# Performance work log

Hardware: AMD Instinct MI355X
Metric: run time of the kernel (lower is better)

The kernel has to match this reference:

```python
import jax, jax.numpy as jnp
import numpy as np

ALPHA = 2.0
BETA = 50.0
BASE = 0.5
MARGIN = 0.1

B, D = 8192, 128
NUM_CLASSES = 512


def setup_inputs() -> dict:
    key = jax.random.key(0)
    k1, k2 = jax.random.split(key)
    emb = jax.random.normal(k1, (B, D), dtype=jnp.float32)
    emb = emb / jnp.linalg.norm(emb, axis=1, keepdims=True)  # unit-norm embeddings (standard for MS loss)
    labels = jax.random.randint(k2, (B,), 0, NUM_CLASSES, dtype=jnp.int64)
    return {"emb": emb, "labels": labels}


def reference(emb, labels):
    # sim: [B, B] similarity matrix
    sim = emb @ emb.T
    n = emb.shape[0]
    eq = labels[:, None] == labels[None, :]
    eye = jnp.eye(n, dtype=bool)
    pos = eq & ~eye          # positive pairs, diagonal removed
    neg = ~eq                # negative pairs

    # per-row hard-mining thresholds
    pos_min = jnp.min(jnp.where(pos, sim, jnp.inf), axis=1)    # min positive sim per row
    neg_max = jnp.max(jnp.where(neg, sim, -jnp.inf), axis=1)   # max negative sim per row

    neg_hard = neg & (sim + MARGIN > pos_min[:, None])
    pos_hard = pos & (sim - MARGIN < neg_max[:, None])

    # fallback: if mining selects nothing in a row, use all pos/neg (matches torch code)
    neg_sel = jnp.where(jnp.any(neg_hard, axis=1, keepdims=True), neg_hard, neg)
    pos_sel = jnp.where(jnp.any(pos_hard, axis=1, keepdims=True), pos_hard, pos)

    pos_loss = jnp.log1p(jnp.sum(jnp.where(pos_sel, jnp.exp(-ALPHA * (sim - BASE)), 0.0), axis=1)) / ALPHA
    neg_loss = jnp.log1p(jnp.sum(jnp.where(neg_sel, jnp.exp(BETA * (sim - BASE)), 0.0), axis=1)) / BETA

    valid = jnp.any(pos, axis=1) & jnp.any(neg, axis=1)  # rows skipped in torch loop
    row_loss = pos_loss + neg_loss
    num_valid = jnp.maximum(jnp.sum(valid.astype(jnp.float32)), 1.0)
    return jnp.sum(jnp.where(valid, row_loss, 0.0)) / num_valid
```

## Files before the change

kernel.cpp:

```cpp
#include <hip/hip_runtime.h>
#include <hip/hip_bf16.h>

#define NROW 8192
#define NDIM 128
#define CTILE 64
#define CCHUNK 8
#define RBLK 128
#define CAP 64
#define NCLS 512

typedef __attribute__((ext_vector_type(8))) short short8;
typedef __attribute__((ext_vector_type(4))) float f32x4;
typedef __attribute__((address_space(1))) const unsigned int guint;
typedef __attribute__((address_space(3))) unsigned int luint;

__device__ __forceinline__ unsigned f2u_mono(float f) {
  unsigned u = __float_as_uint(f);
  return (u & 0x80000000u) ? ~u : (u | 0x80000000u);
}
__device__ __forceinline__ float u2f_mono(unsigned u) {
  return __uint_as_float((u & 0x80000000u) ? (u ^ 0x80000000u) : ~u);
}
__device__ __forceinline__ unsigned short f2bf(float f) {
  unsigned u = __float_as_uint(f);
  u += 0x7fffu + ((u >> 16) & 1u);
  return (unsigned short)(u >> 16);
}

__global__ __launch_bounds__(256) void k_convert(const float* __restrict__ e,
                                                 unsigned short* __restrict__ h,
                                                 const int* __restrict__ labels,
                                                 unsigned* __restrict__ cls_cnt,
                                                 int* __restrict__ cls_list) {
  const int gid = blockIdx.x * 256 + threadIdx.x;
  if (gid < NROW) {
    const int c = labels[gid];
    const unsigned idx = atomicAdd(&cls_cnt[c], 1u);
    if (idx < CAP) cls_list[c * CAP + idx] = gid;
  }
  int i = gid * 8;
  float4 f0 = *reinterpret_cast<const float4*>(e + i);
  float4 f1 = *reinterpret_cast<const float4*>(e + i + 4);
  ushort4 a, b;
  a.x = f2bf(f0.x); a.y = f2bf(f0.y); a.z = f2bf(f0.z); a.w = f2bf(f0.w);
  b.x = f2bf(f1.x); b.y = f2bf(f1.y); b.z = f2bf(f1.z); b.w = f2bf(f1.w);
  *reinterpret_cast<ushort4*>(h + i) = a;
  *reinterpret_cast<ushort4*>(h + i + 4) = b;
}

__global__ __launch_bounds__(256) void k_pos1(
    const float* __restrict__ emb, const unsigned* __restrict__ cls_cnt,
    const int* __restrict__ cls_list, float* __restrict__ pmin,
    float* __restrict__ apb, float* __restrict__ pcache) {
  __shared__ float Le[CAP][NDIM + 1];
  __shared__ int rows_s[CAP];
  const int c = blockIdx.x;
  const int t = threadIdx.x;
  const int cnt = (int)min(cls_cnt[c], (unsigned)CAP);
  if (cnt == 0) return;
  if (t < cnt) rows_s[t] = cls_list[c * CAP + t];
  __syncthreads();
  for (int idx = t; idx < cnt * NDIM; idx += 256) {
    const int k = idx >> 7, d = idx & 127;
    Le[k][d] = emb[(size_t)rows_s[k] * NDIM + d];
  }
  __syncthreads();

  const int il = t >> 4, jl = t & 15;
  for (int ib = 0; ib < cnt; ib += 16) {
    const int i = ib + il;
    float pm = INFINITY, apv = 0.f;
    for (int jb = 0; jb < cnt; jb += 16) {
      const int j = jb + jl;
      float p = INFINITY;
      if (i < cnt && j < cnt) {
        if (i != j) {
          float s = 0.f;
#pragma unroll 8
          for (int d = 0; d < NDIM; ++d) s = fmaf(Le[i][d], Le[j][d], s);
          p = s;
        }
        pcache[(size_t)rows_s[i] * CAP + j] = p;
        if (i != j) {
          pm = fminf(pm, p);
          apv += exp2f(fmaf(p, -2.885390082f, 1.442695041f));
        }
      }
    }
    pm = fminf(pm, __shfl_xor(pm, 1)); pm = fminf(pm, __shfl_xor(pm, 2));
    pm = fminf(pm, __shfl_xor(pm, 4)); pm = fminf(pm, __shfl_xor(pm, 8));
    apv += __shfl_xor(apv, 1); apv += __shfl_xor(apv, 2);
    apv += __shfl_xor(apv, 4); apv += __shfl_xor(apv, 8);
    if (jl == 0 && i < cnt) {
      pmin[rows_s[i]] = pm;
      apb[rows_s[i]] = apv;
    }
  }
}

__device__ __forceinline__ void stage_tile(const unsigned short* __restrict__ eh,
                                           int colBase, int t,
                                           unsigned short* __restrict__ Lbuf) {
#pragma unroll
  for (int it = 0; it < 4; ++it) {
    const int idx = it * 256 + t;
    const int r = idx >> 4;
    const int c = idx & 15;
    const int q = c ^ (r & 15);
    const unsigned short* src = eh + (size_t)(colBase + r) * NDIM + q * 8;
    unsigned short* dst = Lbuf + r * NDIM + c * 8;
    __builtin_amdgcn_global_load_lds((guint*)src, (luint*)dst, 16, 0, 0);
  }
}

__device__ __forceinline__ void mfma_from_lds(const unsigned short* __restrict__ Lbuf,
                                              const short8 (&bv)[4][2],
                                              const f32x4& Z,
                                              int g, int l15,
                                              f32x4 (&acc)[4][2]) {
#pragma unroll
  for (int kk = 0; kk < 4; ++kk) {
    short8 av[4];
#pragma unroll
    for (int m = 0; m < 4; ++m) {
      const int R = m * 16 + l15;
      const int pc = (kk * 4 + g) ^ l15;
      av[m] = *reinterpret_cast<const short8*>(Lbuf + R * NDIM + pc * 8);
    }
#pragma unroll
    for (int m = 0; m < 4; ++m)
#pragma unroll
      for (int n = 0; n < 2; ++n)
        acc[m][n] = __builtin_amdgcn_mfma_f32_16x16x32_bf16(
            av[m], bv[kk][n], (kk == 0) ? Z : acc[m][n], 0, 0, 0);
  }
}

__global__ __launch_bounds__(256, 3) void k_neg(
    const unsigned short* __restrict__ eh, const int* __restrict__ labels,
    const float* __restrict__ pmin, unsigned* __restrict__ nmaxu,
    float* __restrict__ anb, float* __restrict__ hnb) {
  __shared__ unsigned short L[2][CTILE * NDIM];

  const int t = threadIdx.x;
  const int lane = t & 63;
  const int wid = t >> 6;
  const int g = lane >> 4;
  const int l15 = lane & 15;
  const int rowBase = blockIdx.y * RBLK;
  const int col0 = blockIdx.x * CCHUNK * CTILE;

  stage_tile(eh, col0, t, L[0]);

  short8 bv[4][2];
  int lr[2];
  float thrn[2];
#pragma unroll
  for (int n = 0; n < 2; ++n) {
    const int grow = rowBase + wid * 32 + n * 16 + l15;
    lr[n] = labels[grow];
    thrn[n] = pmin[grow] - 0.1f;
#pragma unroll
    for (int kk = 0; kk < 4; ++kk)
      bv[kk][n] = *reinterpret_cast<const short8*>(eh + (size_t)grow * NDIM + kk * 32 + g * 8);
  }

  float nmaxA[2] = {-INFINITY, -INFINITY};
  float anA[2] = {0.f, 0.f}, hnA[2] = {0.f, 0.f};
  const f32x4 Z = {0.f, 0.f, 0.f, 0.f};

  asm volatile("s_waitcnt vmcnt(0)");
  __syncthreads();

  f32x4 acc[4][2];
  int cur = 0;
  for (int tt = 0; tt < CCHUNK; ++tt) {
    const int colBase = col0 + tt * CTILE;
    if (tt + 1 < CCHUNK) stage_tile(eh, colBase + CTILE, t, L[cur ^ 1]);
    int4 lcv[4];
#pragma unroll
    for (int m = 0; m < 4; ++m)
      lcv[m] = *reinterpret_cast<const int4*>(labels + colBase + m * 16 + g * 4);
    mfma_from_lds(L[cur], bv, Z, g, l15, acc);
#pragma unroll
    for (int n = 0; n < 2; ++n) {
#pragma unroll
      for (int m = 0; m < 4; ++m) {
#pragma unroll
        for (int r = 0; r < 4; ++r) {
          const float s = acc[m][n][r];
          const int lc = (r == 0) ? lcv[m].x : (r == 1) ? lcv[m].y
                        : (r == 2) ? lcv[m].z : lcv[m].w;
          const float x = (lr[n] == lc) ? -INFINITY : s;
          nmaxA[n] = fmaxf(nmaxA[n], x);
          const float e = exp2f(fmaf(x, 72.13475205f, -36.06737602f));
          anA[n] += e;
          hnA[n] += (x > thrn[n]) ? e : 0.f;
        }
      }
    }
    asm volatile("s_waitcnt vmcnt(0)");
    __syncthreads();
    cur ^= 1;
  }

#pragma unroll
  for (int n = 0; n < 2; ++n) {
    const int grow = rowBase + wid * 32 + n * 16 + l15;
    float nm = nmaxA[n], a0 = anA[n], a1 = hnA[n];
    nm = fmaxf(nm, __shfl_xor(nm, 16)); nm = fmaxf(nm, __shfl_xor(nm, 32));
    a0 += __shfl_xor(a0, 16); a0 += __shfl_xor(a0, 32);
    a1 += __shfl_xor(a1, 16); a1 += __shfl_xor(a1, 32);
    if (g == 0 && nm > -INFINITY) atomicMax(&nmaxu[grow], f2u_mono(nm));
    if (g == 1 && a0 > 0.f) atomicAdd(&anb[grow], a0);
    if (g == 2 && a1 > 0.f) atomicAdd(&hnb[grow], a1);
  }
}

__global__ __launch_bounds__(256) void k_final(
    const int* __restrict__ labels, const unsigned* __restrict__ cls_cnt,
    const unsigned* __restrict__ nmaxu, const float* __restrict__ pcache,
    const float* __restrict__ apb, const float* __restrict__ anb,
    const float* __restrict__ hnb, float* __restrict__ partial,
    unsigned* __restrict__ done, float* __restrict__ out) {
  const int t = threadIdx.x;
  const int row = blockIdx.x * 256 + t;
  const int c = labels[row];
  const int cnt = (int)min(cls_cnt[c], (unsigned)CAP);
  const float thrp = u2f_mono(nmaxu[row]) + 0.1f;
  float hp = 0.f;
  for (int j = 0; j < cnt; ++j) {
    const float p = pcache[(size_t)row * CAP + j];
    hp += (p < thrp) ? exp2f(fmaf(p, -2.885390082f, 1.442695041f)) : 0.f;
  }
  const float ap = apb[row], an = anb[row], hn = hnb[row];
  const bool valid = (ap > 0.f) && (an > 0.f);
  const float ps = (hp > 0.f) ? hp : ap;
  const float ns = (hn > 0.f) ? hn : an;
  float acc = valid ? (0.5f * log1pf(ps) + 0.02f * log1pf(ns)) : 0.f;
  float cntv = valid ? 1.f : 0.f;
#pragma unroll
  for (int o = 32; o > 0; o >>= 1) {
    acc += __shfl_down(acc, o);
    cntv += __shfl_down(cntv, o);
  }
  __shared__ float sa[4], sc[4];
  const int w = t >> 6, lane = t & 63;
  if (lane == 0) { sa[w] = acc; sc[w] = cntv; }
  __syncthreads();
  if (t == 0) {
    atomicAdd(&partial[0], sa[0] + sa[1] + sa[2] + sa[3]);
    atomicAdd(&partial[1], sc[0] + sc[1] + sc[2] + sc[3]);
    __threadfence();
    if (atomicAdd(done, 1u) == (unsigned)(NROW / 256 - 1)) {
      const float A = atomicAdd(&partial[0], 0.f);
      const float C = atomicAdd(&partial[1], 0.f);
      out[0] = A / fmaxf(C, 1.f);
    }
  }
}

extern "C" void kernel_launch(void* const* d_in, const int* in_sizes, int n_in,
                              void* d_out, int out_size, void* d_ws, size_t ws_size,
                              hipStream_t stream) {
  const float* emb = (const float*)d_in[0];
  const int* labels = (const int*)d_in[1];
  float* out = (float*)d_out;

  unsigned short* embh = (unsigned short*)d_ws;
  float* pmin = (float*)((char*)d_ws + (size_t)NROW * NDIM * 2);
  float* apb = pmin + NROW;
  unsigned* nmaxu = (unsigned*)(apb + NROW);
  float* anb = (float*)(nmaxu + NROW);
  float* hnb = anb + NROW;
  unsigned* cls_cnt = (unsigned*)(hnb + NROW);
  unsigned* done = cls_cnt + NCLS;
  float* partial = (float*)(done + 1);
  int* cls_list = (int*)(partial + 2);
  float* pcache = (float*)(cls_list + NCLS * CAP);

  hipMemsetAsync(nmaxu, 0, (size_t)NROW * 4 * 3 + NCLS * 4 + 12, stream);

  k_convert<<<NROW * NDIM / (256 * 8), 256, 0, stream>>>(emb, embh, labels,
                                                         cls_cnt, cls_list);
  k_pos1<<<NCLS, 256, 0, stream>>>(emb, cls_cnt, cls_list, pmin, apb, pcache);
  dim3 grid(NROW / (CTILE * CCHUNK), NROW / RBLK);
  k_neg<<<grid, 256, 0, stream>>>(embh, labels, pmin, nmaxu, anb, hnb);
  k_final<<<NROW / 256, 256, 0, stream>>>(labels, cls_cnt, nmaxu, pcache,
                                          apb, anb, hnb, partial, done, out);
}
```

Measured before the change: 73.80 us.

## Fuse memset, bf16 conversion and class bucketing into per-class positive kernel

Drops the memset and the separate convert kernel. A single per-class kernel now zeroes the accumulators, converts a slice of embeddings to bf16, and builds its class member list by scanning all labels with shared-memory atomics. Per-row class counts are written to a new buffer so the final kernel no longer reads labels or class counts. This removes two launches and the global atomic bucketing, at the cost of every block scanning all 8192 labels.

```diff
diff --git a/kernel.cpp b/kernel.cpp
--- a/kernel.cpp
+++ b/kernel.cpp
@@ -27,39 +27,52 @@
   return (unsigned short)(u >> 16);
 }
 
-__global__ __launch_bounds__(256) void k_convert(const float* __restrict__ e,
-                                                 unsigned short* __restrict__ h,
-                                                 const int* __restrict__ labels,
-                                                 unsigned* __restrict__ cls_cnt,
-                                                 int* __restrict__ cls_list) {
-  const int gid = blockIdx.x * 256 + threadIdx.x;
-  if (gid < NROW) {
-    const int c = labels[gid];
-    const unsigned idx = atomicAdd(&cls_cnt[c], 1u);
-    if (idx < CAP) cls_list[c * CAP + idx] = gid;
-  }
-  int i = gid * 8;
-  float4 f0 = *reinterpret_cast<const float4*>(e + i);
-  float4 f1 = *reinterpret_cast<const float4*>(e + i + 4);
-  ushort4 a, b;
-  a.x = f2bf(f0.x); a.y = f2bf(f0.y); a.z = f2bf(f0.z); a.w = f2bf(f0.w);
-  b.x = f2bf(f1.x); b.y = f2bf(f1.y); b.z = f2bf(f1.z); b.w = f2bf(f1.w);
-  *reinterpret_cast<ushort4*>(h + i) = a;
-  *reinterpret_cast<ushort4*>(h + i + 4) = b;
-}
-
-__global__ __launch_bounds__(256) void k_pos1(
-    const float* __restrict__ emb, const unsigned* __restrict__ cls_cnt,
-    const int* __restrict__ cls_list, float* __restrict__ pmin,
-    float* __restrict__ apb, float* __restrict__ pcache) {
+__global__ __launch_bounds__(256) void k_pre(
+    const float* __restrict__ emb, const int* __restrict__ labels,
+    unsigned short* __restrict__ h,
+    unsigned* __restrict__ nmaxu, float* __restrict__ anb, float* __restrict__ hnb,
+    float* __restrict__ pmin, float* __restrict__ apb, int* __restrict__ rcnt,
+    float* __restrict__ pcache, unsigned* __restrict__ done_partial) {
   __shared__ float Le[CAP][NDIM + 1];
   __shared__ int rows_s[CAP];
+  __shared__ int scnt;
+
+  const int t = threadIdx.x;
   const int c = blockIdx.x;
-  const int t = threadIdx.x;
-  const int cnt = (int)min(cls_cnt[c], (unsigned)CAP);
+  const int gid = c * 256 + t;
+
+  if (gid < NROW) {
+    nmaxu[gid] = 0u;
+    anb[gid] = 0.f;
+    hnb[gid] = 0.f;
+  }
+  if (c == 0 && t < 3) done_partial[t] = 0u;
+
+  {
+    int i = gid * 8;
+    float4 f0 = *reinterpret_cast<const float4*>(emb + i);
+    float4 f1 = *reinterpret_cast<const float4*>(emb + i + 4);
+    ushort4 a, b;
+    a.x = f2bf(f0.x); a.y = f2bf(f0.y); a.z = f2bf(f0.z); a.w = f2bf(f0.w);
+    b.x = f2bf(f1.x); b.y = f2bf(f1.y); b.z = f2bf(f1.z); b.w = f2bf(f1.w);
+    *reinterpret_cast<ushort4*>(h + i) = a;
+    *reinterpret_cast<ushort4*>(h + i + 4) = b;
+  }
+
+  if (t == 0) scnt = 0;
+  __syncthreads();
+#pragma unroll
+  for (int it = 0; it < NROW / 256; ++it) {
+    const int row = it * 256 + t;
+    if (labels[row] == c) {
+      const int idx = atomicAdd(&scnt, 1);
+      if (idx < CAP) rows_s[idx] = row;
+    }
+  }
+  __syncthreads();
+  const int cnt = min(scnt, CAP);
   if (cnt == 0) return;
-  if (t < cnt) rows_s[t] = cls_list[c * CAP + t];
-  __syncthreads();
+
   for (int idx = t; idx < cnt * NDIM; idx += 256) {
     const int k = idx >> 7, d = idx & 127;
     Le[k][d] = emb[(size_t)rows_s[k] * NDIM + d];
@@ -94,6 +107,7 @@
     if (jl == 0 && i < cnt) {
       pmin[rows_s[i]] = pm;
       apb[rows_s[i]] = apv;
+      rcnt[rows_s[i]] = cnt;
     }
   }
 }
@@ -218,15 +232,15 @@
 }
 
 __global__ __launch_bounds__(256) void k_final(
-    const int* __restrict__ labels, const unsigned* __restrict__ cls_cnt,
-    const unsigned* __restrict__ nmaxu, const float* __restrict__ pcache,
-    const float* __restrict__ apb, const float* __restrict__ anb,
-    const float* __restrict__ hnb, float* __restrict__ partial,
-    unsigned* __restrict__ done, float* __restrict__ out) {
+    const int* __restrict__ rcnt, const unsigned* __restrict__ nmaxu,
+    const float* __restrict__ pcache, const float* __restrict__ apb,
+    const float* __restrict__ anb, const float* __restrict__ hnb,
+    unsigned* __restrict__ done_partial, float* __restrict__ out) {
+  unsigned* done = done_partial;
+  float* partial = (float*)(done_partial + 1);
   const int t = threadIdx.x;
   const int row = blockIdx.x * 256 + t;
-  const int c = labels[row];
-  const int cnt = (int)min(cls_cnt[c], (unsigned)CAP);
+  const int cnt = min(rcnt[row], CAP);
   const float thrp = u2f_mono(nmaxu[row]) + 0.1f;
   float hp = 0.f;
   for (int j = 0; j < cnt; ++j) {
@@ -273,19 +287,14 @@
   unsigned* nmaxu = (unsigned*)(apb + NROW);
   float* anb = (float*)(nmaxu + NROW);
   float* hnb = anb + NROW;
-  unsigned* cls_cnt = (unsigned*)(hnb + NROW);
-  unsigned* done = cls_cnt + NCLS;
-  float* partial = (float*)(done + 1);
-  int* cls_list = (int*)(partial + 2);
-  float* pcache = (float*)(cls_list + NCLS * CAP);
-
-  hipMemsetAsync(nmaxu, 0, (size_t)NROW * 4 * 3 + NCLS * 4 + 12, stream);
-
-  k_convert<<<NROW * NDIM / (256 * 8), 256, 0, stream>>>(emb, embh, labels,
-                                                         cls_cnt, cls_list);
-  k_pos1<<<NCLS, 256, 0, stream>>>(emb, cls_cnt, cls_list, pmin, apb, pcache);
+  int* rcnt = (int*)(hnb + NROW);
+  unsigned* done_partial = (unsigned*)(rcnt + NROW);
+  float* pcache = (float*)(done_partial + 4);
+
+  k_pre<<<NCLS, 256, 0, stream>>>(emb, labels, embh, nmaxu, anb, hnb,
+                                  pmin, apb, rcnt, pcache, done_partial);
   dim3 grid(NROW / (CTILE * CCHUNK), NROW / RBLK);
   k_neg<<<grid, 256, 0, stream>>>(embh, labels, pmin, nmaxu, anb, hnb);
-  k_final<<<NROW / 256, 256, 0, stream>>>(labels, cls_cnt, nmaxu, pcache,
-                                          apb, anb, hnb, partial, done, out);
-}
+  k_final<<<NROW / 256, 256, 0, stream>>>(rcnt, nmaxu, pcache,
+                                          apb, anb, hnb, done_partial, out);
+}
```

Result: faster. 66.68 us (-9.6%).
